# Kernel tuning notes

Measured on AMD Instinct MI355X. Metric: run time of the kernel, lower is better.

## Reference

```python
import jax, jax.numpy as jnp
import numpy as np

B, S, D = 2, 2048, 1024   # batch, seq, d_model
E, F, K = 8, 2048, 2      # num_experts, ffn_hidden_size, top_k


def setup_inputs() -> dict:
    key = jax.random.key(0)
    ks = jax.random.split(key, 5)
    scale = 0.02
    hidden_states = jax.random.normal(ks[0], (B, S, D), dtype=jnp.float32)
    router_kernel = jax.random.normal(ks[1], (D, E), dtype=jnp.float32) * scale
    # expert params, already reshaped to (E, F, D) as in DbrxExpertGLU.expert_shape
    w1 = jax.random.normal(ks[2], (E, F, D), dtype=jnp.float32) * scale
    v1 = jax.random.normal(ks[3], (E, F, D), dtype=jnp.float32) * scale
    w2 = jax.random.normal(ks[4], (E, F, D), dtype=jnp.float32) * scale
    return {"hidden_states": hidden_states, "router_kernel": router_kernel,
            "w1": w1, "v1": v1, "w2": w2}


def reference(hidden_states, router_kernel, w1, v1, w2):
    # ---- Router ----
    logits = jnp.einsum('bsd,de->bse', hidden_states.astype(jnp.float32), router_kernel)
    weights = jax.nn.softmax(logits, axis=-1)                # [B,S,E]
    top_weights, top_experts = jax.lax.top_k(weights, K)     # [B,S,K]
    # moe_normalize_expert_weights = 1 -> L1 normalization
    top_weights = top_weights / jnp.sum(jnp.abs(top_weights), axis=-1, keepdims=True)
    weights = weights.astype(hidden_states.dtype)
    top_weights = top_weights.astype(hidden_states.dtype)
    # ---- Experts: every expert's GLU over all tokens, masked accumulation ----
    out = jnp.zeros_like(hidden_states)
    for e in range(E):  # small fixed expert count; matches original loop
        x1 = jnp.einsum('bsd,fd->bsf', hidden_states, w1[e])   # [B,S,F]
        x2 = jnp.einsum('bsd,fd->bsf', hidden_states, v1[e])
        h = jax.nn.silu(x1) * x2
        y_e = jnp.einsum('bsf,fd->bsd', h, w2[e])               # [B,S,D]
        gate = jnp.sum((top_experts == e) * top_weights, axis=-1)  # [B,S]
        out = out + gate[:, :, None] * y_e
    return out, weights
```

## Files before the change

kernel.cpp:

```cpp
#include <hip/hip_runtime.h>
#include <stdint.h>
#include <math.h>

#define NB 2
#define NS 2048
#define ND 1024
#define NE 8
#define NF 2048
#define NTOK (NB*NS)
#define EFD ((size_t)NE*NF*ND)

typedef short bf16x8 __attribute__((ext_vector_type(8)));
typedef float f32x4 __attribute__((ext_vector_type(4)));

__device__ __forceinline__ unsigned short f2bf(float f) {
  unsigned u = __float_as_uint(f);
  unsigned r = (u + 0x7FFFu + ((u >> 16) & 1u)) >> 16;
  return (unsigned short)r;
}

__device__ __forceinline__ void async16(unsigned short* lds, const unsigned short* g) {
  __builtin_amdgcn_global_load_lds(
      (const __attribute__((address_space(1))) unsigned int*)g,
      (__attribute__((address_space(3))) unsigned int*)lds, 16, 0, 0);
}

#define VMCNT(n) asm volatile("s_waitcnt vmcnt(" #n ")" ::: "memory")
#define LGKM0    asm volatile("s_waitcnt lgkmcnt(0)" ::: "memory")
#define SBAR     __builtin_amdgcn_s_barrier()
#define SCHED0   __builtin_amdgcn_sched_barrier(0)

__global__ void cvt_bf16(const float* __restrict__ src,
                         unsigned short* __restrict__ dst, int n4) {
  int i = blockIdx.x * blockDim.x + threadIdx.x;
  int stride = gridDim.x * blockDim.x;
  for (; i < n4; i += stride) {
    float4 v = ((const float4*)src)[i];
    ushort4 o;
    o.x = f2bf(v.x); o.y = f2bf(v.y); o.z = f2bf(v.z); o.w = f2bf(v.w);
    ((ushort4*)dst)[i] = o;
  }
}

__global__ void transpose_w2(const float* __restrict__ w2,
                             unsigned short* __restrict__ w2t) {
  __shared__ float tile[32][33];
  int e = blockIdx.z;
  int d0 = blockIdx.x * 32, f0 = blockIdx.y * 32;
  int tx = threadIdx.x, ty = threadIdx.y;
  const float* src = w2 + (size_t)e * NF * ND;
  unsigned short* dst = w2t + (size_t)e * ND * NF;
#pragma unroll
  for (int i = ty; i < 32; i += 8)
    tile[i][tx] = src[(size_t)(f0 + i) * ND + d0 + tx];
  __syncthreads();
#pragma unroll
  for (int i = ty; i < 32; i += 8)
    dst[(size_t)(d0 + i) * NF + f0 + tx] = f2bf(tile[tx][i]);
}

__global__ void router_kernel(const float* __restrict__ hs,
                              const float* __restrict__ rk,
                              float* __restrict__ wout,
                              float* __restrict__ tw,
                              int* __restrict__ choice,
                              unsigned short* __restrict__ hsb) {
  int lane = threadIdx.x;
  int tt = lane & 15, part = lane >> 4;
  int t = blockIdx.x * 16 + tt;
  const float4* hrow = (const float4*)(hs + (size_t)t * ND) + part * 64;
  ushort4* hb4 = (ushort4*)(hsb + (size_t)t * ND) + part * 64;
  const float4* rk4 = (const float4*)rk + part * 512;
  float acc[NE];
#pragma unroll
  for (int e = 0; e < NE; ++e) acc[e] = 0.f;
#pragma unroll 4
  for (int i = 0; i < 64; ++i) {
    float4 x = hrow[i];
    ushort4 o;
    o.x = f2bf(x.x); o.y = f2bf(x.y); o.z = f2bf(x.z); o.w = f2bf(x.w);
    hb4[i] = o;
    float xs[4] = {x.x, x.y, x.z, x.w};
#pragma unroll
    for (int j = 0; j < 4; ++j) {
      float4 r0 = rk4[i * 8 + j * 2];
      float4 r1 = rk4[i * 8 + j * 2 + 1];
      acc[0] += xs[j] * r0.x; acc[1] += xs[j] * r0.y;
      acc[2] += xs[j] * r0.z; acc[3] += xs[j] * r0.w;
      acc[4] += xs[j] * r1.x; acc[5] += xs[j] * r1.y;
      acc[6] += xs[j] * r1.z; acc[7] += xs[j] * r1.w;
    }
  }
#pragma unroll
  for (int e = 0; e < NE; ++e) {
    acc[e] += __shfl_xor(acc[e], 16, 64);
    acc[e] += __shfl_xor(acc[e], 32, 64);
  }
  if (part == 0) {
    float mx = acc[0]; int i0 = 0;
#pragma unroll
    for (int e = 1; e < NE; ++e) if (acc[e] > mx) { mx = acc[e]; i0 = e; }
    float m2 = -3.4e38f; int i1 = 0;
#pragma unroll
    for (int e = 0; e < NE; ++e) if (e != i0 && acc[e] > m2) { m2 = acc[e]; i1 = e; }
    float p[NE]; float den = 0.f;
#pragma unroll
    for (int e = 0; e < NE; ++e) { p[e] = expf(acc[e] - mx); den += p[e]; }
    float inv = 1.f / den;
#pragma unroll
    for (int e = 0; e < NE; ++e) { p[e] *= inv; wout[t * NE + e] = p[e]; }
    float w0 = p[i0], w1 = p[i1];
    float s = 1.f / (w0 + w1);
    tw[t * 2 + 0] = w0 * s;
    tw[t * 2 + 1] = w1 * s;
    choice[t] = i0 | (i1 << 4);
  }
}

__global__ void build_lists(const int* __restrict__ choice,
                            int* __restrict__ counts,
                            int* __restrict__ list) {
  __shared__ int lcnt[NE];
  int tid = threadIdx.x;
  if (tid < NE) lcnt[tid] = 0;
  __syncthreads();
  int4 c4 = ((const int4*)choice)[tid];
  int cs[4] = {c4.x, c4.y, c4.z, c4.w};
#pragma unroll
  for (int j = 0; j < 4; ++j) {
    int t = tid * 4 + j;
    int e0 = cs[j] & 15, e1 = (cs[j] >> 4) & 15;
    int p0 = atomicAdd(&lcnt[e0], 1);
    list[e0 * NTOK + p0] = t << 1;
    int p1 = atomicAdd(&lcnt[e1], 1);
    list[e1 * NTOK + p1] = (t << 1) | 1;
  }
  __syncthreads();
  if (tid < NE) counts[tid] = lcnt[tid];
}

__global__ __launch_bounds__(256, 2) void gemm_fused(
    const int* __restrict__ counts, const int* __restrict__ list,
    const unsigned short* __restrict__ A,
    const unsigned short* __restrict__ B1,
    const unsigned short* __restrict__ B2,
    unsigned short* __restrict__ H) {
  int bid = blockIdx.x;
  int e = bid >> 9;
  int rem = bid & 511;
  int mt = rem >> 4, nt = rem & 15;
  int cnt = counts[e];
  if (mt * 128 >= cnt) return;

  __shared__ unsigned short lds[3][12288];

  int tid = threadIdx.x;
  int wid = tid >> 6, lane = tid & 63;
  int wr = wid >> 1, wc = wid & 1;
  int l15 = lane & 15, l4 = lane >> 4;
  const int* mylist = list + e * NTOK;

  int trow = tid >> 2;
  int co = ((tid & 3) ^ ((tid >> 3) & 3)) * 8;
  const unsigned short* aS0;
  const unsigned short* aS1;
  {
    int r0 = mt * 128 + trow;
    int r1 = r0 + 64;
    if (r0 >= cnt) r0 = cnt - 1;
    if (r1 >= cnt) r1 = cnt - 1;
    int e0 = mylist[r0], e1 = mylist[r1];
    aS0 = A + (size_t)(e0 >> 1) * ND + co;
    aS1 = A + (size_t)(e1 >> 1) * ND + co;
  }
  const unsigned short* b1S0 = B1 + (size_t)e * NF * ND + (size_t)(nt * 128 + trow) * ND + co;
  const unsigned short* b1S1 = b1S0 + (size_t)64 * ND;
  const unsigned short* b2S0 = B2 + (size_t)e * NF * ND + (size_t)(nt * 128 + trow) * ND + co;
  const unsigned short* b2S1 = b2S0 + (size_t)64 * ND;

  int rowA[4], rowB[4];
#pragma unroll
  for (int mi = 0; mi < 4; ++mi) {
    int r = wr * 64 + mi * 16 + l15;
    rowA[mi] = r * 64 + ((l4 ^ ((r >> 1) & 3)) << 4);
  }
#pragma unroll
  for (int ni = 0; ni < 4; ++ni) {
    int r = wc * 64 + ni * 16 + l15;
    rowB[ni] = r * 64 + ((l4 ^ ((r >> 1) & 3)) << 4);
  }

  f32x4 acc1[4][4], acc2[4][4];
#pragma unroll
  for (int mi = 0; mi < 4; ++mi)
#pragma unroll
    for (int ni = 0; ni < 4; ++ni) {
      f32x4 z = {0.f, 0.f, 0.f, 0.f};
      acc1[mi][ni] = z; acc2[mi][ni] = z;
    }

  auto STAGE = [&](int c, int kt) {
    int ko = kt * 32;
    unsigned short* base = &lds[c][0] + tid * 8;
    async16(base,         aS0 + ko);
    async16(base + 2048,  aS1 + ko);
    async16(base + 4096,  b1S0 + ko);
    async16(base + 6144,  b1S1 + ko);
    async16(base + 8192,  b2S0 + ko);
    async16(base + 10240, b2S1 + ko);
  };

  const int kT = ND / 32;
  STAGE(0, 0); STAGE(1, 1); STAGE(2, 2);

  int cur = 0;
  for (int kt = 0; kt < kT; ++kt) {
    if (kt + 2 < kT)      { VMCNT(12); }
    else if (kt + 1 < kT) { VMCNT(6); }
    else                  { VMCNT(0); }
    SCHED0;
    SBAR;

    const char* la = (const char*)&lds[cur][0];
    const char* lb1 = la + 8192;
    const char* lb2 = la + 16384;
    bf16x8 a[4], b1[4], b2[4];
#pragma unroll
    for (int mi = 0; mi < 4; ++mi)
      a[mi] = *(const bf16x8*)(la + rowA[mi]);
#pragma unroll
    for (int ni = 0; ni < 4; ++ni) {
      b1[ni] = *(const bf16x8*)(lb1 + rowB[ni]);
      b2[ni] = *(const bf16x8*)(lb2 + rowB[ni]);
    }
    LGKM0;
    SCHED0;
    SBAR;
    if (kt + 3 < kT) STAGE(cur, kt + 3);

    __builtin_amdgcn_s_setprio(1);
#pragma unroll
    for (int mi = 0; mi < 4; ++mi)
#pragma unroll
      for (int ni = 0; ni < 4; ++ni) {
        acc1[mi][ni] = __builtin_amdgcn_mfma_f32_16x16x32_bf16(
            a[mi], b1[ni], acc1[mi][ni], 0, 0, 0);
        acc2[mi][ni] = __builtin_amdgcn_mfma_f32_16x16x32_bf16(
            a[mi], b2[ni], acc2[mi][ni], 0, 0, 0);
      }
    __builtin_amdgcn_s_setprio(0);

    cur = (cur == 2) ? 0 : cur + 1;
  }

  int rowbase = mt * 128 + wr * 64;
  int colbase = nt * 128 + wc * 64;
#pragma unroll
  for (int mi = 0; mi < 4; ++mi) {
#pragma unroll
    for (int j = 0; j < 4; ++j) {
      int r = rowbase + mi * 16 + l4 * 4 + j;
      if (r >= cnt) continue;
      int entry = mylist[r];
      long crow = (long)(entry & 1) * NTOK + (entry >> 1);
#pragma unroll
      for (int ni = 0; ni < 4; ++ni) {
        int c = colbase + ni * 16 + l15;
        float x1 = acc1[mi][ni][j];
        float x2 = acc2[mi][ni][j];
        float h = (x1 / (1.f + expf(-x1))) * x2;
        H[crow * (long)NF + c] = f2bf(h);
      }
    }
  }
}

__global__ __launch_bounds__(256, 2) void gemm_p3(
    const int* __restrict__ counts, const int* __restrict__ list,
    const unsigned short* __restrict__ Ah,
    const unsigned short* __restrict__ Bw,
    float* __restrict__ Y) {
  int bid = blockIdx.x;
  int e = bid >> 8;
  int rem = bid & 255;
  int mt = rem >> 3;
  int code = rem & 7;
  int nt = code >> 1, kh = code & 1;
  int cnt = counts[e];
  if (mt * 128 >= cnt) return;

  __shared__ unsigned short lds[3][12288];

  int tid = threadIdx.x;
  int wid = tid >> 6, lane = tid & 63;
  int wr = wid >> 1, wc = wid & 1;
  int l15 = lane & 15, l4 = lane >> 4;
  const int* mylist = list + e * NTOK;

  int trow = tid >> 2;
  int co = ((tid & 3) ^ ((tid >> 3) & 3)) * 8;
  const unsigned short* aS[2];
#pragma unroll
  for (int g = 0; g < 2; ++g) {
    int r = mt * 128 + g * 64 + trow;
    if (r >= cnt) r = cnt - 1;
    int entry = mylist[r];
    long crow = (long)(entry & 1) * NTOK + (entry >> 1);
    aS[g] = Ah + crow * (long)NF + kh * 1024 + co;
  }
  const unsigned short* bS[4];
#pragma unroll
  for (int g = 0; g < 4; ++g) {
    int d = nt * 256 + g * 64 + trow;
    bS[g] = Bw + (size_t)e * ND * NF + (size_t)d * NF + kh * 1024 + co;
  }

  int rowA[4], rowB[8];
#pragma unroll
  for (int mi = 0; mi < 4; ++mi) {
    int r = wr * 64 + mi * 16 + l15;
    rowA[mi] = r * 64 + ((l4 ^ ((r >> 1) & 3)) << 4);
  }
#pragma unroll
  for (int ni = 0; ni < 8; ++ni) {
    int r = wc * 128 + ni * 16 + l15;
    rowB[ni] = 8192 + r * 64 + ((l4 ^ ((r >> 1) & 3)) << 4);
  }

  f32x4 acc[4][8];
#pragma unroll
  for (int mi = 0; mi < 4; ++mi)
#pragma unroll
    for (int ni = 0; ni < 8; ++ni) {
      f32x4 z = {0.f, 0.f, 0.f, 0.f};
      acc[mi][ni] = z;
    }

  auto STAGE = [&](int c, int kt) {
    int ko = kt * 32;
    unsigned short* base = &lds[c][0] + tid * 8;
    async16(base,         aS[0] + ko);
    async16(base + 2048,  aS[1] + ko);
    async16(base + 4096,  bS[0] + ko);
    async16(base + 6144,  bS[1] + ko);
    async16(base + 8192,  bS[2] + ko);
    async16(base + 10240, bS[3] + ko);
  };

  const int kT = 32;
  STAGE(0, 0); STAGE(1, 1); STAGE(2, 2);

  int cur = 0;
  for (int kt = 0; kt < kT; ++kt) {
    if (kt + 2 < kT)      { VMCNT(12); }
    else if (kt + 1 < kT) { VMCNT(6); }
    else                  { VMCNT(0); }
    SCHED0;
    SBAR;

    const char* buf = (const char*)&lds[cur][0];
    bf16x8 a[4], b[8];
#pragma unroll
    for (int mi = 0; mi < 4; ++mi)
      a[mi] = *(const bf16x8*)(buf + rowA[mi]);
#pragma unroll
    for (int ni = 0; ni < 8; ++ni)
      b[ni] = *(const bf16x8*)(buf + rowB[ni]);
    LGKM0;
    SCHED0;
    SBAR;
    if (kt + 3 < kT) STAGE(cur, kt + 3);

    __builtin_amdgcn_s_setprio(1);
#pragma unroll
    for (int mi = 0; mi < 4; ++mi)
#pragma unroll
      for (int ni = 0; ni < 8; ++ni)
        acc[mi][ni] = __builtin_amdgcn_mfma_f32_16x16x32_bf16(
            a[mi], b[ni], acc[mi][ni], 0, 0, 0);
    __builtin_amdgcn_s_setprio(0);

    cur = (cur == 2) ? 0 : cur + 1;
  }

  float* Yp = Y + (size_t)kh * 2 * NTOK * ND;
#pragma unroll
  for (int mi = 0; mi < 4; ++mi)
#pragma unroll
    for (int j = 0; j < 4; ++j) {
      int r = mt * 128 + wr * 64 + mi * 16 + l4 * 4 + j;
      if (r >= cnt) continue;
      int entry = mylist[r];
      long crow = (long)(entry & 1) * NTOK + (entry >> 1);
#pragma unroll
      for (int ni = 0; ni < 8; ++ni) {
        int d = nt * 256 + wc * 128 + ni * 16 + l15;
        Yp[crow * (long)ND + d] = acc[mi][ni][j];
      }
    }
}

__global__ void combine_kernel(const float* __restrict__ ybuf,
                               const float* __restrict__ tw,
                               float* __restrict__ out) {
  const int S4 = NTOK * ND / 4;
  const int KH4 = 2 * NTOK * ND / 4;
  int i = blockIdx.x * blockDim.x + threadIdx.x;
  int stride = gridDim.x * blockDim.x;
  const float4* yb = (const float4*)ybuf;
  for (; i < S4; i += stride) {
    int t = i >> 8;
    float w0 = tw[t * 2], w1 = tw[t * 2 + 1];
    float4 a0 = yb[i], b0 = yb[i + KH4];
    float4 a1 = yb[i + S4], b1 = yb[i + S4 + KH4];
    float4 o;
    o.x = w0 * (a0.x + b0.x) + w1 * (a1.x + b1.x);
    o.y = w0 * (a0.y + b0.y) + w1 * (a1.y + b1.y);
    o.z = w0 * (a0.z + b0.z) + w1 * (a1.z + b1.z);
    o.w = w0 * (a0.w + b0.w) + w1 * (a1.w + b1.w);
    ((float4*)out)[i] = o;
  }
}


extern "C" void kernel_launch(void* const* d_in, const int* in_sizes, int n_in,
                              void* d_out, int out_size, void* d_ws, size_t ws_size,
                              hipStream_t stream) {
  const float* hs = (const float*)d_in[0];
  const float* rk = (const float*)d_in[1];
  const float* w1 = (const float*)d_in[2];
  const float* v1 = (const float*)d_in[3];
  const float* w2 = (const float*)d_in[4];
  float* out = (float*)d_out;
  float* wout = out + (size_t)NTOK * ND;

  char* ws = (char*)d_ws;
  int* counts = (int*)(ws + 0);
  int* list = (int*)(ws + 256);
  float* tw = (float*)(ws + 131328);
  int* choice = (int*)(ws + 164096);
  unsigned short* hsb = (unsigned short*)(ws + 180480);
  unsigned short* w1b = (unsigned short*)(ws + 8569088);
  unsigned short* v1b = (unsigned short*)(ws + 42123520);
  unsigned short* w2t = (unsigned short*)(ws + 75677952);
  unsigned short* hbuf = (unsigned short*)(ws + 109232384);
  float* ybuf = (float*)(ws + 142786816);

  router_kernel<<<256, 64, 0, stream>>>(hs, rk, wout, tw, choice, hsb);
  build_lists<<<1, 1024, 0, stream>>>(choice, counts, list);

  cvt_bf16<<<4096, 256, 0, stream>>>(w1, w1b, (int)(EFD / 4));
  cvt_bf16<<<4096, 256, 0, stream>>>(v1, v1b, (int)(EFD / 4));
  transpose_w2<<<dim3(ND / 32, NF / 32, NE), dim3(32, 8), 0, stream>>>(w2, w2t);

  gemm_fused<<<4096, 256, 0, stream>>>(counts, list, hsb, w1b, v1b, hbuf);

  gemm_p3<<<2048, 256, 0, stream>>>(counts, list, hbuf, w2t, ybuf);

  combine_kernel<<<2048, 256, 0, stream>>>(ybuf, tw, out);
}
```

Measured before the change: 287.3 us.

## Store intermediates in compact expert-sorted order and use bf16 partial outputs

The GLU intermediate H and the down-projection partials Y are now written in a compact layout sorted by expert, using per-expert offsets, instead of being scattered by token index. This removes the gather through the list from gemm_p3's A loads and makes its row reads contiguous. Y partials are stored as bf16 rather than fp32, which halves the bytes written and then read back. The combine kernel now gathers each token's two expert rows through a new position table. The cost is lower precision in the partial sums and an extra position array.

```diff
diff --git a/kernel.cpp b/kernel.cpp
--- a/kernel.cpp
+++ b/kernel.cpp
@@ -9,6 +9,7 @@
 #define NF 2048
 #define NTOK (NB*NS)
 #define EFD ((size_t)NE*NF*ND)
+#define NROWS (2*NTOK)
 
 typedef short bf16x8 __attribute__((ext_vector_type(8)));
 typedef float f32x4 __attribute__((ext_vector_type(4)));
@@ -17,6 +18,9 @@
   unsigned u = __float_as_uint(f);
   unsigned r = (u + 0x7FFFu + ((u >> 16) & 1u)) >> 16;
   return (unsigned short)r;
+}
+__device__ __forceinline__ float bf2f(unsigned short s) {
+  return __uint_as_float(((unsigned)s) << 16);
 }
 
 __device__ __forceinline__ void async16(unsigned short* lds, const unsigned short* g) {
@@ -119,7 +123,9 @@
 
 __global__ void build_lists(const int* __restrict__ choice,
                             int* __restrict__ counts,
-                            int* __restrict__ list) {
+                            int* __restrict__ off,
+                            int* __restrict__ list,
+                            int* __restrict__ posn) {
   __shared__ int lcnt[NE];
   int tid = threadIdx.x;
   if (tid < NE) lcnt[tid] = 0;
@@ -134,13 +140,20 @@
     list[e0 * NTOK + p0] = t << 1;
     int p1 = atomicAdd(&lcnt[e1], 1);
     list[e1 * NTOK + p1] = (t << 1) | 1;
+    posn[t] = p0 | (p1 << 16);
   }
   __syncthreads();
-  if (tid < NE) counts[tid] = lcnt[tid];
+  if (tid == 0) {
+    int s = 0;
+#pragma unroll
+    for (int e = 0; e < NE; ++e) { counts[e] = lcnt[e]; off[e] = s; s += lcnt[e]; }
+    off[NE] = s;
+  }
 }
 
 __global__ __launch_bounds__(256, 2) void gemm_fused(
-    const int* __restrict__ counts, const int* __restrict__ list,
+    const int* __restrict__ counts, const int* __restrict__ off,
+    const int* __restrict__ list,
     const unsigned short* __restrict__ A,
     const unsigned short* __restrict__ B1,
     const unsigned short* __restrict__ B2,
@@ -151,6 +164,7 @@
   int mt = rem >> 4, nt = rem & 15;
   int cnt = counts[e];
   if (mt * 128 >= cnt) return;
+  int off_e = off[e];
 
   __shared__ unsigned short lds[3][12288];
 
@@ -261,25 +275,24 @@
     for (int j = 0; j < 4; ++j) {
       int r = rowbase + mi * 16 + l4 * 4 + j;
       if (r >= cnt) continue;
-      int entry = mylist[r];
-      long crow = (long)(entry & 1) * NTOK + (entry >> 1);
+      size_t row = (size_t)(off_e + r);
 #pragma unroll
       for (int ni = 0; ni < 4; ++ni) {
         int c = colbase + ni * 16 + l15;
         float x1 = acc1[mi][ni][j];
         float x2 = acc2[mi][ni][j];
         float h = (x1 / (1.f + expf(-x1))) * x2;
-        H[crow * (long)NF + c] = f2bf(h);
+        H[row * NF + c] = f2bf(h);
       }
     }
   }
 }
 
 __global__ __launch_bounds__(256, 2) void gemm_p3(
-    const int* __restrict__ counts, const int* __restrict__ list,
+    const int* __restrict__ counts, const int* __restrict__ off,
     const unsigned short* __restrict__ Ah,
     const unsigned short* __restrict__ Bw,
-    float* __restrict__ Y) {
+    unsigned short* __restrict__ Y) {
   int bid = blockIdx.x;
   int e = bid >> 8;
   int rem = bid & 255;
@@ -288,6 +301,7 @@
   int nt = code >> 1, kh = code & 1;
   int cnt = counts[e];
   if (mt * 128 >= cnt) return;
+  int off_e = off[e];
 
   __shared__ unsigned short lds[3][12288];
 
@@ -295,7 +309,6 @@
   int wid = tid >> 6, lane = tid & 63;
   int wr = wid >> 1, wc = wid & 1;
   int l15 = lane & 15, l4 = lane >> 4;
-  const int* mylist = list + e * NTOK;
 
   int trow = tid >> 2;
   int co = ((tid & 3) ^ ((tid >> 3) & 3)) * 8;
@@ -304,9 +317,7 @@
   for (int g = 0; g < 2; ++g) {
     int r = mt * 128 + g * 64 + trow;
     if (r >= cnt) r = cnt - 1;
-    int entry = mylist[r];
-    long crow = (long)(entry & 1) * NTOK + (entry >> 1);
-    aS[g] = Ah + crow * (long)NF + kh * 1024 + co;
+    aS[g] = Ah + (size_t)(off_e + r) * NF + kh * 1024 + co;
   }
   const unsigned short* bS[4];
 #pragma unroll
@@ -383,43 +394,47 @@
     cur = (cur == 2) ? 0 : cur + 1;
   }
 
-  float* Yp = Y + (size_t)kh * 2 * NTOK * ND;
+  unsigned short* Yp = Y + (size_t)kh * NROWS * ND;
 #pragma unroll
   for (int mi = 0; mi < 4; ++mi)
 #pragma unroll
     for (int j = 0; j < 4; ++j) {
       int r = mt * 128 + wr * 64 + mi * 16 + l4 * 4 + j;
       if (r >= cnt) continue;
-      int entry = mylist[r];
-      long crow = (long)(entry & 1) * NTOK + (entry >> 1);
+      size_t row = (size_t)(off_e + r);
 #pragma unroll
       for (int ni = 0; ni < 8; ++ni) {
         int d = nt * 256 + wc * 128 + ni * 16 + l15;
-        Yp[crow * (long)ND + d] = acc[mi][ni][j];
+        Yp[row * ND + d] = f2bf(acc[mi][ni][j]);
       }
     }
 }
 
-__global__ void combine_kernel(const float* __restrict__ ybuf,
+__global__ void combine_kernel(const unsigned short* __restrict__ yc,
                                const float* __restrict__ tw,
+                               const int* __restrict__ choice,
+                               const int* __restrict__ posn,
+                               const int* __restrict__ off,
                                float* __restrict__ out) {
-  const int S4 = NTOK * ND / 4;
-  const int KH4 = 2 * NTOK * ND / 4;
-  int i = blockIdx.x * blockDim.x + threadIdx.x;
-  int stride = gridDim.x * blockDim.x;
-  const float4* yb = (const float4*)ybuf;
-  for (; i < S4; i += stride) {
-    int t = i >> 8;
-    float w0 = tw[t * 2], w1 = tw[t * 2 + 1];
-    float4 a0 = yb[i], b0 = yb[i + KH4];
-    float4 a1 = yb[i + S4], b1 = yb[i + S4 + KH4];
-    float4 o;
-    o.x = w0 * (a0.x + b0.x) + w1 * (a1.x + b1.x);
-    o.y = w0 * (a0.y + b0.y) + w1 * (a1.y + b1.y);
-    o.z = w0 * (a0.z + b0.z) + w1 * (a1.z + b1.z);
-    o.w = w0 * (a0.w + b0.w) + w1 * (a1.w + b1.w);
-    ((float4*)out)[i] = o;
-  }
+  int t = blockIdx.x;
+  int tid = threadIdx.x;
+  int ch = choice[t];
+  int pp = posn[t];
+  int e0 = ch & 15, e1 = (ch >> 4) & 15;
+  size_t r0 = (size_t)(off[e0] + (pp & 0xffff));
+  size_t r1 = (size_t)(off[e1] + (pp >> 16));
+  float w0 = tw[t * 2], w1 = tw[t * 2 + 1];
+  const size_t P = (size_t)NROWS * ND;
+  ushort4 a0 = ((const ushort4*)(yc + r0 * ND))[tid];
+  ushort4 b0 = ((const ushort4*)(yc + P + r0 * ND))[tid];
+  ushort4 a1 = ((const ushort4*)(yc + r1 * ND))[tid];
+  ushort4 b1 = ((const ushort4*)(yc + P + r1 * ND))[tid];
+  float4 o;
+  o.x = w0 * (bf2f(a0.x) + bf2f(b0.x)) + w1 * (bf2f(a1.x) + bf2f(b1.x));
+  o.y = w0 * (bf2f(a0.y) + bf2f(b0.y)) + w1 * (bf2f(a1.y) + bf2f(b1.y));
+  o.z = w0 * (bf2f(a0.z) + bf2f(b0.z)) + w1 * (bf2f(a1.z) + bf2f(b1.z));
+  o.w = w0 * (bf2f(a0.w) + bf2f(b0.w)) + w1 * (bf2f(a1.w) + bf2f(b1.w));
+  ((float4*)(out + (size_t)t * ND))[tid] = o;
 }
 
 
@@ -436,26 +451,28 @@
 
   char* ws = (char*)d_ws;
   int* counts = (int*)(ws + 0);
-  int* list = (int*)(ws + 256);
-  float* tw = (float*)(ws + 131328);
-  int* choice = (int*)(ws + 164096);
-  unsigned short* hsb = (unsigned short*)(ws + 180480);
-  unsigned short* w1b = (unsigned short*)(ws + 8569088);
-  unsigned short* v1b = (unsigned short*)(ws + 42123520);
-  unsigned short* w2t = (unsigned short*)(ws + 75677952);
-  unsigned short* hbuf = (unsigned short*)(ws + 109232384);
-  float* ybuf = (float*)(ws + 142786816);
+  int* off = (int*)(ws + 64);
+  int* choice = (int*)(ws + 128);
+  int* posn = (int*)(ws + 16512);
+  float* tw = (float*)(ws + 32896);
+  int* list = (int*)(ws + 65664);
+  unsigned short* hsb = (unsigned short*)(ws + 196736);
+  unsigned short* w1b = (unsigned short*)(ws + 8585344);
+  unsigned short* v1b = (unsigned short*)(ws + 42139776);
+  unsigned short* w2t = (unsigned short*)(ws + 75694208);
+  unsigned short* hcomp = (unsigned short*)(ws + 109248640);
+  unsigned short* ycomp = (unsigned short*)(ws + 142803072);
 
   router_kernel<<<256, 64, 0, stream>>>(hs, rk, wout, tw, choice, hsb);
-  build_lists<<<1, 1024, 0, stream>>>(choice, counts, list);
+  build_lists<<<1, 1024, 0, stream>>>(choice, counts, off, list, posn);
 
   cvt_bf16<<<4096, 256, 0, stream>>>(w1, w1b, (int)(EFD / 4));
   cvt_bf16<<<4096, 256, 0, stream>>>(v1, v1b, (int)(EFD / 4));
   transpose_w2<<<dim3(ND / 32, NF / 32, NE), dim3(32, 8), 0, stream>>>(w2, w2t);
 
-  gemm_fused<<<4096, 256, 0, stream>>>(counts, list, hsb, w1b, v1b, hbuf);
-
-  gemm_p3<<<2048, 256, 0, stream>>>(counts, list, hbuf, w2t, ybuf);
-
-  combine_kernel<<<2048, 256, 0, stream>>>(ybuf, tw, out);
-}
+  gemm_fused<<<4096, 256, 0, stream>>>(counts, off, list, hsb, w1b, v1b, hcomp);
+
+  gemm_p3<<<2048, 256, 0, stream>>>(counts, off, hcomp, w2t, ycomp);
+
+  combine_kernel<<<NTOK, 256, 0, stream>>>(ycomp, tw, choice, posn, off, out);
+}
```

After: 273.2 us. 4.9% less time.
